# Optimization experiments

Measured on AMD Instinct MI355X. Metric: run time of the kernel, lower is better.

Reference implementation:

```python
import jax, jax.numpy as jnp
import numpy as np

NUM_CATS = 5
EPS = 1e-6


def setup_inputs() -> dict:
    key = jax.random.key(0)
    k1, k2, k3, k4 = jax.random.split(key, 4)
    B, C, H, W = 64, 3, 256, 256
    restored = jax.random.normal(k1, (B, C, H, W), dtype=jnp.float32)
    clean_patch_1 = jax.random.normal(k2, (B, C, H, W), dtype=jnp.float32)
    un = jax.random.uniform(k3, (B, C, H, W), dtype=jnp.float32)
    de_id = jax.random.randint(k4, (B,), 0, NUM_CATS)
    return {"restored": restored, "clean_patch_1": clean_patch_1,
            "de_id": de_id, "un": un}


def _loss(restored, clean, un, de_id):
    B, C, H, W = restored.shape
    E = C * H * W  # elements per sample
    dt = restored.dtype

    onehot = (de_id[:, None] == jnp.arange(NUM_CATS)[None, :])  # [B,5] bool
    m = onehot.astype(dt)                                        # [B,5]
    counts = onehot.sum(0)                                       # [5] int
    nonempty = counts > 0
    safe_counts = jnp.maximum(counts, 1).astype(dt)              # avoid 0-div

    # Per-category mean uncertainty map: un_map[c] = mean_{i: de_id[i]=c} un[i] + eps
    un_sum = jnp.einsum('bk,bchw->kchw', m, un)                  # [5,C,H,W]
    un_map = un_sum / safe_counts[:, None, None, None] + EPS     # [5,C,H,W]
    s = 1.0 / un_map                                             # [5,C,H,W]

    # Per-sample scaled L1 (s gathered by each sample's category)
    absdiff = jnp.abs(clean - restored)                          # [B,C,H,W]
    scaled_sum_per_sample = (absdiff * s[de_id]).sum(axis=(1, 2, 3))  # [B]
    abs_sum_per_sample = absdiff.sum(axis=(1, 2, 3))                  # [B]

    cat_scaled_sum = jnp.einsum('bk,b->k', m, scaled_sum_per_sample)  # [5]
    cat_abs_sum = jnp.einsum('bk,b->k', m, abs_sum_per_sample)        # [5]

    # NOTE: the original code never clears un_hq_list/un_lq_list between
    # categories, so the L1 at category c is the mean over ALL samples from
    # categories 0..c (each scaled by its OWN category's s). Replicate that
    # via cumulative sums/counts over the category axis.
    cum_scaled = jnp.cumsum(cat_scaled_sum)                      # [5]
    cum_elems = jnp.cumsum(counts).astype(dt) * E                # [5]
    cum_l1 = cum_scaled / jnp.maximum(cum_elems, 1.0)            # [5]

    old_loss = jnp.where(nonempty, cat_abs_sum / (safe_counts * E), 0.0)
    un_num = un_map.mean(axis=(1, 2, 3))                         # [5]
    bn = jnp.where(nonempty, 2.0 * jnp.log(un_num), 0.0)
    unc_l1 = jnp.where(nonempty, cum_l1, 0.0)

    cat_losses = unc_l1 + bn                                     # [5]
    num = nonempty.sum().astype(dt)
    total = cat_losses.sum() / num
    return total, cat_losses, old_loss, bn, unc_l1


def reference(restored, clean_patch_1, de_id, un):
    return _loss(restored, clean_patch_1, un, de_id)
```

## Files before the change

kernel.cpp:

```cpp
#include <hip/hip_runtime.h>
#include <math.h>

#define NCAT  5
#define BATCH 64
#define ELEMS 196608
#define P4    49152
#define EPSV  1e-6f

#define P1_TPB 64
#define P1_NBLK 768
#define P1_GRP 8

#define P2_PB  192
#define P2_SCH 8
#define P2_CHB (BATCH / P2_SCH)
#define P2_NCOL (P2_PB * P2_SCH)

#define NBLK 768
#define TPB  256
#define GRP  8

__global__ __launch_bounds__(P1_TPB) void phase1_kernel(
    const float4* __restrict__ un,
    const int*    __restrict__ de_id,
    float4*       __restrict__ rmap,
    float*        __restrict__ partials1)
{
    __shared__ int   sh_de[BATCH];
    __shared__ float sh_inv[NCAT];

    const int tid = threadIdx.x;
    {
        int k = de_id[tid];
        sh_de[tid] = k;
        #pragma unroll
        for (int j = 0; j < NCAT; ++j) {
            unsigned long long m = __ballot(k == j);
            if (tid == j) {
                int c = __popcll(m);
                sh_inv[j] = 1.0f / (float)(c > 0 ? c : 1);
            }
        }
    }
    __syncthreads();

    const int p4 = blockIdx.x * P1_TPB + tid;
    const float4* up = un + p4;

    float4 un_s[NCAT];
    #pragma unroll
    for (int j = 0; j < NCAT; ++j) un_s[j] = make_float4(0.f, 0.f, 0.f, 0.f);

    float4 ub[2][P1_GRP];
    #pragma unroll
    for (int i = 0; i < P1_GRP; ++i) ub[0][i] = up[(size_t)i * P4];

    #pragma unroll
    for (int g = 0; g < BATCH / P1_GRP; ++g) {
        const int cur = g & 1, nxt = cur ^ 1;
        if (g < BATCH / P1_GRP - 1) {
            #pragma unroll
            for (int i = 0; i < P1_GRP; ++i)
                ub[nxt][i] = up[(size_t)((g + 1) * P1_GRP + i) * P4];
        }
        #pragma unroll
        for (int i = 0; i < P1_GRP; ++i) {
            float4 u = ub[cur][i];
            int k = sh_de[g * P1_GRP + i];
            #pragma unroll
            for (int j = 0; j < NCAT; ++j) {
                float m = (k == j) ? 1.0f : 0.0f;
                un_s[j].x = fmaf(m, u.x, un_s[j].x);
                un_s[j].y = fmaf(m, u.y, un_s[j].y);
                un_s[j].z = fmaf(m, u.z, un_s[j].z);
                un_s[j].w = fmaf(m, u.w, un_s[j].w);
            }
        }
    }

    float vals[NCAT];
    #pragma unroll
    for (int j = 0; j < NCAT; ++j) {
        float inv = sh_inv[j];
        float4 r;
        r.x = 1.0f / fmaf(un_s[j].x, inv, EPSV);
        r.y = 1.0f / fmaf(un_s[j].y, inv, EPSV);
        r.z = 1.0f / fmaf(un_s[j].z, inv, EPSV);
        r.w = 1.0f / fmaf(un_s[j].w, inv, EPSV);
        rmap[(size_t)j * P4 + p4] = r;
        vals[j] = un_s[j].x + un_s[j].y + un_s[j].z + un_s[j].w;
    }

    #pragma unroll
    for (int j = 0; j < NCAT; ++j) {
        float v = vals[j];
        #pragma unroll
        for (int off = 32; off >= 1; off >>= 1)
            v += __shfl_down(v, off, 64);
        if (tid == 0) partials1[j * P1_NBLK + blockIdx.x] = v;
    }
}

__global__ __launch_bounds__(256) void phase2_kernel(
    const float4* __restrict__ restored,
    const float4* __restrict__ clean,
    const int*    __restrict__ de_id,
    const float4* __restrict__ rmap,
    float*        __restrict__ partials2)
{
    __shared__ int   sh_de[BATCH];
    __shared__ float sred[4][2 * NCAT];

    const int tid = threadIdx.x;
    if (tid < 64) sh_de[tid] = de_id[tid];
    __syncthreads();

    const int p4 = blockIdx.x * 256 + tid;
    const int b0 = blockIdx.y * P2_CHB;
    const float4* cp = clean + p4;
    const float4* rp = restored + p4;

    float4 ad4[NCAT];
    #pragma unroll
    for (int j = 0; j < NCAT; ++j) ad4[j] = make_float4(0.f, 0.f, 0.f, 0.f);

    float4 cb[2][2], rb[2][2];
    #pragma unroll
    for (int i = 0; i < 2; ++i) {
        const size_t off = (size_t)(b0 + i) * P4;
        cb[0][i] = cp[off];
        rb[0][i] = rp[off];
    }

    #pragma unroll
    for (int g = 0; g < P2_CHB / 2; ++g) {
        const int cur = g & 1, nxt = cur ^ 1;
        if (g < P2_CHB / 2 - 1) {
            #pragma unroll
            for (int i = 0; i < 2; ++i) {
                const size_t off = (size_t)(b0 + (g + 1) * 2 + i) * P4;
                cb[nxt][i] = cp[off];
                rb[nxt][i] = rp[off];
            }
        }
        #pragma unroll
        for (int i = 0; i < 2; ++i) {
            float4 c = cb[cur][i], r = rb[cur][i];
            float ax = fabsf(c.x - r.x);
            float ay = fabsf(c.y - r.y);
            float az = fabsf(c.z - r.z);
            float aw = fabsf(c.w - r.w);
            int k = sh_de[b0 + g * 2 + i];
            #pragma unroll
            for (int j = 0; j < NCAT; ++j) {
                float m = (k == j) ? 1.0f : 0.0f;
                ad4[j].x = fmaf(m, ax, ad4[j].x);
                ad4[j].y = fmaf(m, ay, ad4[j].y);
                ad4[j].z = fmaf(m, az, ad4[j].z);
                ad4[j].w = fmaf(m, aw, ad4[j].w);
            }
        }
    }

    float vals[2 * NCAT];
    #pragma unroll
    for (int j = 0; j < NCAT; ++j) {
        float4 m4 = rmap[(size_t)j * P4 + p4];
        vals[j] = ad4[j].x * m4.x + ad4[j].y * m4.y +
                  ad4[j].z * m4.z + ad4[j].w * m4.w;
        vals[NCAT + j] = ad4[j].x + ad4[j].y + ad4[j].z + ad4[j].w;
    }

    #pragma unroll
    for (int i = 0; i < 2 * NCAT; ++i) {
        float v = vals[i];
        #pragma unroll
        for (int off = 32; off >= 1; off >>= 1)
            v += __shfl_down(v, off, 64);
        vals[i] = v;
    }

    const int wave = tid >> 6, lane = tid & 63;
    if (lane == 0) {
        #pragma unroll
        for (int i = 0; i < 2 * NCAT; ++i) sred[wave][i] = vals[i];
    }
    __syncthreads();

    if (tid < 2 * NCAT) {
        float v = sred[0][tid] + sred[1][tid] + sred[2][tid] + sred[3][tid];
        const int col = blockIdx.y * P2_PB + blockIdx.x;
        partials2[tid * P2_NCOL + col] = v;
    }
}

__global__ __launch_bounds__(TPB) void accum_kernel(
    const float* __restrict__ restored,
    const float* __restrict__ clean,
    const int*   __restrict__ de_id,
    const float* __restrict__ un,
    float*       __restrict__ partials)
{
    __shared__ int   sh_de[BATCH];
    __shared__ float sh_inv[NCAT];
    __shared__ float sred[TPB / 64][3 * NCAT];

    const int tid = threadIdx.x;
    if (tid < 64) {
        int k = de_id[tid];
        sh_de[tid] = k;
        #pragma unroll
        for (int j = 0; j < NCAT; ++j) {
            unsigned long long m = __ballot(k == j);
            if (tid == j) {
                int c = __popcll(m);
                sh_inv[j] = 1.0f / (float)(c > 0 ? c : 1);
            }
        }
    }
    __syncthreads();

    const int p = blockIdx.x * TPB + tid;
    const float* rp = restored + p;
    const float* cp = clean + p;
    const float* up = un + p;

    float un_s[NCAT] = {0.f, 0.f, 0.f, 0.f, 0.f};
    float ad_s[NCAT] = {0.f, 0.f, 0.f, 0.f, 0.f};

    float ub[2][GRP], cb[2][GRP], rb[2][GRP];
    #pragma unroll
    for (int i = 0; i < GRP; ++i) {
        const size_t off = (size_t)i * ELEMS;
        ub[0][i] = up[off]; cb[0][i] = cp[off]; rb[0][i] = rp[off];
    }
    #pragma unroll
    for (int g = 0; g < BATCH / GRP; ++g) {
        const int cur = g & 1, nxt = cur ^ 1;
        if (g < BATCH / GRP - 1) {
            #pragma unroll
            for (int i = 0; i < GRP; ++i) {
                const size_t off = (size_t)((g + 1) * GRP + i) * ELEMS;
                ub[nxt][i] = up[off]; cb[nxt][i] = cp[off]; rb[nxt][i] = rp[off];
            }
        }
        #pragma unroll
        for (int i = 0; i < GRP; ++i) {
            float u  = ub[cur][i];
            float ad = fabsf(cb[cur][i] - rb[cur][i]);
            int   k  = sh_de[g * GRP + i];
            #pragma unroll
            for (int j = 0; j < NCAT; ++j) {
                float m = (k == j) ? 1.0f : 0.0f;
                un_s[j] = fmaf(m, u,  un_s[j]);
                ad_s[j] = fmaf(m, ad, ad_s[j]);
            }
        }
    }

    float vals[3 * NCAT];
    #pragma unroll
    for (int j = 0; j < NCAT; ++j) {
        float um = fmaf(un_s[j], sh_inv[j], EPSV);
        vals[j]            = ad_s[j] / um;
        vals[NCAT + j]     = ad_s[j];
        vals[2 * NCAT + j] = un_s[j];
    }
    #pragma unroll
    for (int i = 0; i < 3 * NCAT; ++i) {
        float v = vals[i];
        #pragma unroll
        for (int off = 32; off >= 1; off >>= 1)
            v += __shfl_down(v, off, 64);
        vals[i] = v;
    }
    const int wave = tid >> 6, lane = tid & 63;
    if (lane == 0) {
        #pragma unroll
        for (int i = 0; i < 3 * NCAT; ++i) sred[wave][i] = vals[i];
    }
    __syncthreads();
    if (tid < 3 * NCAT) {
        float v = sred[0][tid] + sred[1][tid] + sred[2][tid] + sred[3][tid];
        partials[tid * NBLK + blockIdx.x] = v;
    }
}

__global__ __launch_bounds__(256) void epilogue_kernel(
    const int*   __restrict__ de_id,
    const float* __restrict__ pSA, int nA,
    const float* __restrict__ pUN, int nB,
    float*       __restrict__ out)
{
    __shared__ int   sh_cnt[NCAT];
    __shared__ float sh_acc[3 * NCAT];

    const int tid = threadIdx.x;
    if (tid < 64) {
        int k = de_id[tid];
        #pragma unroll
        for (int j = 0; j < NCAT; ++j) {
            unsigned long long m = __ballot(k == j);
            if (tid == j) sh_cnt[j] = __popcll(m);
        }
    }

    if (tid < 240) {
        const int row    = tid >> 4;
        const int lane16 = tid & 15;
        const float* base = (row < 10) ? (pSA + row * nA) : (pUN + (row - 10) * nB);
        const int n = (row < 10) ? nA : nB;
        float v = 0.f;
        for (int k = lane16; k < n; k += 16) v += base[k];
        v += __shfl_down(v, 8, 16);
        v += __shfl_down(v, 4, 16);
        v += __shfl_down(v, 2, 16);
        v += __shfl_down(v, 1, 16);
        if (lane16 == 0) sh_acc[row] = v;
    }
    __syncthreads();

    if (tid == 0) {
        const float Ef = (float)ELEMS;
        float cum_s = 0.f;
        long  cum_c = 0;
        float total = 0.f;
        int   num   = 0;
        float cat_losses[NCAT], old_loss[NCAT], bn[NCAT], unc_l1[NCAT];

        for (int j = 0; j < NCAT; ++j) {
            cum_s += sh_acc[j];
            cum_c += sh_cnt[j];
            float cum_elems = (float)cum_c * Ef;
            float cum_l1    = cum_s / fmaxf(cum_elems, 1.0f);

            bool  ne   = sh_cnt[j] > 0;
            float safe = (float)(ne ? sh_cnt[j] : 1);

            old_loss[j]  = ne ? sh_acc[NCAT + j] / (safe * Ef) : 0.f;
            float un_num = sh_acc[2 * NCAT + j] / (safe * Ef) + EPSV;
            bn[j]        = ne ? 2.0f * logf(un_num) : 0.f;
            unc_l1[j]    = ne ? cum_l1 : 0.f;
            cat_losses[j] = unc_l1[j] + bn[j];
            total += cat_losses[j];
            num   += ne ? 1 : 0;
        }
        total /= (float)num;

        out[0] = total;
        for (int j = 0; j < NCAT; ++j) {
            out[1 + j]  = cat_losses[j];
            out[6 + j]  = old_loss[j];
            out[11 + j] = bn[j];
            out[16 + j] = unc_l1[j];
        }
    }
}

extern "C" void kernel_launch(void* const* d_in, const int* in_sizes, int n_in,
                              void* d_out, int out_size, void* d_ws, size_t ws_size,
                              hipStream_t stream) {
    (void)in_sizes; (void)n_in; (void)out_size;
    const float* restored = (const float*)d_in[0];
    const float* clean    = (const float*)d_in[1];
    const int*   de_id    = (const int*)d_in[2];
    const float* un       = (const float*)d_in[3];
    float* out = (float*)d_out;

    const size_t rmap_bytes = (size_t)NCAT * P4 * sizeof(float4);
    const size_t p1_bytes   = (size_t)NCAT * P1_NBLK * sizeof(float);
    const size_t p2_bytes   = (size_t)2 * NCAT * P2_NCOL * sizeof(float);

    if (ws_size >= rmap_bytes + p1_bytes + p2_bytes) {
        float4* rmap      = (float4*)d_ws;
        float*  partials1 = (float*)((char*)d_ws + rmap_bytes);
        float*  partials2 = (float*)((char*)d_ws + rmap_bytes + p1_bytes);

        phase1_kernel<<<P1_NBLK, P1_TPB, 0, stream>>>(
            (const float4*)un, de_id, rmap, partials1);
        phase2_kernel<<<dim3(P2_PB, P2_SCH), 256, 0, stream>>>(
            (const float4*)restored, (const float4*)clean, de_id,
            (const float4*)rmap, partials2);
        epilogue_kernel<<<1, 256, 0, stream>>>(
            de_id, partials2, P2_NCOL, partials1, P1_NBLK, out);
    } else {
        float* partials = (float*)d_ws;
        accum_kernel<<<NBLK, TPB, 0, stream>>>(restored, clean, de_id, un, partials);
        epilogue_kernel<<<1, 256, 0, stream>>>(
            de_id, partials, NBLK, partials + 10 * NBLK, NBLK, out);
    }
}
```

Baseline: 190.1 us.

## Split uncertainty reduction across batch chunks with separate reciprocal-map kernel

The per-category uncertainty sum was computed by 768 single-wave blocks that each walked all 64 samples. It is now split into 8 batch-chunk blocks per position tile, which write per-chunk partial maps. A new kernel sums those partials and forms the reciprocal map. The abs-diff pass is retiled so each thread handles two float4 positions per batch chunk. This exposes more parallelism to hide memory latency, at the cost of writing and re-reading the partial maps in the workspace and one extra kernel launch.

```diff
diff --git a/kernel.cpp b/kernel.cpp
--- a/kernel.cpp
+++ b/kernel.cpp
@@ -7,32 +7,115 @@
 #define P4    49152
 #define EPSV  1e-6f
 
-#define P1_TPB 64
-#define P1_NBLK 768
-#define P1_GRP 8
-
-#define P2_PB  192
-#define P2_SCH 8
-#define P2_CHB (BATCH / P2_SCH)
-#define P2_NCOL (P2_PB * P2_SCH)
+#define TILE4 512
+#define NPOSB 96
+#define BCH   8
+#define NCH   8
+#define NCOLS (NPOSB * NCH)
 
 #define NBLK 768
 #define TPB  256
 #define GRP  8
 
-__global__ __launch_bounds__(P1_TPB) void phase1_kernel(
+__device__ __forceinline__ float hsum4(const float4 v) {
+    return v.x + v.y + v.z + v.w;
+}
+__device__ __forceinline__ float dot4(const float4 a, const float4 b) {
+    return a.x * b.x + a.y * b.y + a.z * b.z + a.w * b.w;
+}
+
+__global__ __launch_bounds__(256) void un_pass_kernel(
     const float4* __restrict__ un,
     const int*    __restrict__ de_id,
-    float4*       __restrict__ rmap,
-    float*        __restrict__ partials1)
+    float4*       __restrict__ unpart,
+    float*        __restrict__ unblk)
 {
-    __shared__ int   sh_de[BATCH];
+    __shared__ int   sh_de[BCH];
+    __shared__ float sred[4][NCAT];
+
+    const int tid = threadIdx.x;
+    const int pb  = blockIdx.x;
+    const int ch  = blockIdx.y;
+    if (tid < BCH) sh_de[tid] = de_id[ch * BCH + tid];
+    __syncthreads();
+
+    const int p0 = pb * TILE4 + tid;
+    const float4* up = un + p0;
+
+    float4 un_s[2][NCAT];
+    #pragma unroll
+    for (int s = 0; s < 2; ++s)
+        #pragma unroll
+        for (int j = 0; j < NCAT; ++j)
+            un_s[s][j] = make_float4(0.f, 0.f, 0.f, 0.f);
+
+    float4 ub[2][2];
+    #pragma unroll
+    for (int s = 0; s < 2; ++s)
+        ub[0][s] = up[(size_t)(ch * BCH) * P4 + (s << 8)];
+
+    #pragma unroll
+    for (int b = 0; b < BCH; ++b) {
+        const int cur = b & 1, nxt = cur ^ 1;
+        if (b < BCH - 1) {
+            #pragma unroll
+            for (int s = 0; s < 2; ++s)
+                ub[nxt][s] = up[(size_t)(ch * BCH + b + 1) * P4 + (s << 8)];
+        }
+        const int k = sh_de[b];
+        #pragma unroll
+        for (int j = 0; j < NCAT; ++j) {
+            const float m = (k == j) ? 1.0f : 0.0f;
+            #pragma unroll
+            for (int s = 0; s < 2; ++s) {
+                un_s[s][j].x = fmaf(m, ub[cur][s].x, un_s[s][j].x);
+                un_s[s][j].y = fmaf(m, ub[cur][s].y, un_s[s][j].y);
+                un_s[s][j].z = fmaf(m, ub[cur][s].z, un_s[s][j].z);
+                un_s[s][j].w = fmaf(m, ub[cur][s].w, un_s[s][j].w);
+            }
+        }
+    }
+
+    #pragma unroll
+    for (int j = 0; j < NCAT; ++j)
+        #pragma unroll
+        for (int s = 0; s < 2; ++s)
+            unpart[(size_t)(ch * NCAT + j) * P4 + p0 + (s << 8)] = un_s[s][j];
+
+    float vals[NCAT];
+    #pragma unroll
+    for (int j = 0; j < NCAT; ++j)
+        vals[j] = hsum4(un_s[0][j]) + hsum4(un_s[1][j]);
+
+    #pragma unroll
+    for (int j = 0; j < NCAT; ++j) {
+        float v = vals[j];
+        #pragma unroll
+        for (int off = 32; off >= 1; off >>= 1)
+            v += __shfl_down(v, off, 64);
+        vals[j] = v;
+    }
+    const int wave = tid >> 6, lane = tid & 63;
+    if (lane == 0) {
+        #pragma unroll
+        for (int j = 0; j < NCAT; ++j) sred[wave][j] = vals[j];
+    }
+    __syncthreads();
+    if (tid < NCAT) {
+        float v = sred[0][tid] + sred[1][tid] + sred[2][tid] + sred[3][tid];
+        unblk[tid * NCOLS + ch * NPOSB + pb] = v;
+    }
+}
+
+__global__ __launch_bounds__(256) void rmap_kernel(
+    const int*    __restrict__ de_id,
+    const float4* __restrict__ unpart,
+    float4*       __restrict__ rmap)
+{
     __shared__ float sh_inv[NCAT];
-
     const int tid = threadIdx.x;
-    {
+    if (tid < 64) {
         int k = de_id[tid];
-        sh_de[tid] = k;
         #pragma unroll
         for (int j = 0; j < NCAT; ++j) {
             unsigned long long m = __ballot(k == j);
@@ -44,120 +127,84 @@
     }
     __syncthreads();
 
-    const int p4 = blockIdx.x * P1_TPB + tid;
-    const float4* up = un + p4;
-
-    float4 un_s[NCAT];
-    #pragma unroll
-    for (int j = 0; j < NCAT; ++j) un_s[j] = make_float4(0.f, 0.f, 0.f, 0.f);
-
-    float4 ub[2][P1_GRP];
-    #pragma unroll
-    for (int i = 0; i < P1_GRP; ++i) ub[0][i] = up[(size_t)i * P4];
-
-    #pragma unroll
-    for (int g = 0; g < BATCH / P1_GRP; ++g) {
-        const int cur = g & 1, nxt = cur ^ 1;
-        if (g < BATCH / P1_GRP - 1) {
-            #pragma unroll
-            for (int i = 0; i < P1_GRP; ++i)
-                ub[nxt][i] = up[(size_t)((g + 1) * P1_GRP + i) * P4];
-        }
-        #pragma unroll
-        for (int i = 0; i < P1_GRP; ++i) {
-            float4 u = ub[cur][i];
-            int k = sh_de[g * P1_GRP + i];
-            #pragma unroll
-            for (int j = 0; j < NCAT; ++j) {
-                float m = (k == j) ? 1.0f : 0.0f;
-                un_s[j].x = fmaf(m, u.x, un_s[j].x);
-                un_s[j].y = fmaf(m, u.y, un_s[j].y);
-                un_s[j].z = fmaf(m, u.z, un_s[j].z);
-                un_s[j].w = fmaf(m, u.w, un_s[j].w);
-            }
-        }
-    }
-
-    float vals[NCAT];
-    #pragma unroll
-    for (int j = 0; j < NCAT; ++j) {
-        float inv = sh_inv[j];
-        float4 r;
-        r.x = 1.0f / fmaf(un_s[j].x, inv, EPSV);
-        r.y = 1.0f / fmaf(un_s[j].y, inv, EPSV);
-        r.z = 1.0f / fmaf(un_s[j].z, inv, EPSV);
-        r.w = 1.0f / fmaf(un_s[j].w, inv, EPSV);
-        rmap[(size_t)j * P4 + p4] = r;
-        vals[j] = un_s[j].x + un_s[j].y + un_s[j].z + un_s[j].w;
-    }
-
-    #pragma unroll
-    for (int j = 0; j < NCAT; ++j) {
-        float v = vals[j];
-        #pragma unroll
-        for (int off = 32; off >= 1; off >>= 1)
-            v += __shfl_down(v, off, 64);
-        if (tid == 0) partials1[j * P1_NBLK + blockIdx.x] = v;
-    }
-}
-
-__global__ __launch_bounds__(256) void phase2_kernel(
+    const int p4  = blockIdx.x * 256 + tid;
+    const int cat = blockIdx.y;
+
+    float4 s = make_float4(0.f, 0.f, 0.f, 0.f);
+    #pragma unroll
+    for (int ch = 0; ch < NCH; ++ch) {
+        float4 v = unpart[(size_t)(ch * NCAT + cat) * P4 + p4];
+        s.x += v.x; s.y += v.y; s.z += v.z; s.w += v.w;
+    }
+    const float inv = sh_inv[cat];
+    float4 r;
+    r.x = 1.0f / fmaf(s.x, inv, EPSV);
+    r.y = 1.0f / fmaf(s.y, inv, EPSV);
+    r.z = 1.0f / fmaf(s.z, inv, EPSV);
+    r.w = 1.0f / fmaf(s.w, inv, EPSV);
+    rmap[(size_t)cat * P4 + p4] = r;
+}
+
+__global__ __launch_bounds__(256) void ad_pass_kernel(
     const float4* __restrict__ restored,
     const float4* __restrict__ clean,
+    const float4* __restrict__ rmap,
     const int*    __restrict__ de_id,
-    const float4* __restrict__ rmap,
-    float*        __restrict__ partials2)
+    float*        __restrict__ part2)
 {
-    __shared__ int   sh_de[BATCH];
+    __shared__ int   sh_de[BCH];
     __shared__ float sred[4][2 * NCAT];
 
     const int tid = threadIdx.x;
-    if (tid < 64) sh_de[tid] = de_id[tid];
-    __syncthreads();
-
-    const int p4 = blockIdx.x * 256 + tid;
-    const int b0 = blockIdx.y * P2_CHB;
-    const float4* cp = clean + p4;
-    const float4* rp = restored + p4;
-
-    float4 ad4[NCAT];
-    #pragma unroll
-    for (int j = 0; j < NCAT; ++j) ad4[j] = make_float4(0.f, 0.f, 0.f, 0.f);
+    const int pb  = blockIdx.x;
+    const int ch  = blockIdx.y;
+    if (tid < BCH) sh_de[tid] = de_id[ch * BCH + tid];
+    __syncthreads();
+
+    const int p0 = pb * TILE4 + tid;
+    const float4* cp = clean + p0;
+    const float4* rp = restored + p0;
+
+    float4 ad_s[2][NCAT];
+    #pragma unroll
+    for (int s = 0; s < 2; ++s)
+        #pragma unroll
+        for (int j = 0; j < NCAT; ++j)
+            ad_s[s][j] = make_float4(0.f, 0.f, 0.f, 0.f);
 
     float4 cb[2][2], rb[2][2];
     #pragma unroll
-    for (int i = 0; i < 2; ++i) {
-        const size_t off = (size_t)(b0 + i) * P4;
-        cb[0][i] = cp[off];
-        rb[0][i] = rp[off];
-    }
-
-    #pragma unroll
-    for (int g = 0; g < P2_CHB / 2; ++g) {
-        const int cur = g & 1, nxt = cur ^ 1;
-        if (g < P2_CHB / 2 - 1) {
-            #pragma unroll
-            for (int i = 0; i < 2; ++i) {
-                const size_t off = (size_t)(b0 + (g + 1) * 2 + i) * P4;
-                cb[nxt][i] = cp[off];
-                rb[nxt][i] = rp[off];
-            }
-        }
-        #pragma unroll
-        for (int i = 0; i < 2; ++i) {
-            float4 c = cb[cur][i], r = rb[cur][i];
-            float ax = fabsf(c.x - r.x);
-            float ay = fabsf(c.y - r.y);
-            float az = fabsf(c.z - r.z);
-            float aw = fabsf(c.w - r.w);
-            int k = sh_de[b0 + g * 2 + i];
+    for (int s = 0; s < 2; ++s) {
+        const size_t off = (size_t)(ch * BCH) * P4 + (s << 8);
+        cb[0][s] = cp[off];
+        rb[0][s] = rp[off];
+    }
+
+    #pragma unroll
+    for (int b = 0; b < BCH; ++b) {
+        const int cur = b & 1, nxt = cur ^ 1;
+        if (b < BCH - 1) {
+            #pragma unroll
+            for (int s = 0; s < 2; ++s) {
+                const size_t off = (size_t)(ch * BCH + b + 1) * P4 + (s << 8);
+                cb[nxt][s] = cp[off];
+                rb[nxt][s] = rp[off];
+            }
+        }
+        const int k = sh_de[b];
+        #pragma unroll
+        for (int s = 0; s < 2; ++s) {
+            float ax = fabsf(cb[cur][s].x - rb[cur][s].x);
+            float ay = fabsf(cb[cur][s].y - rb[cur][s].y);
+            float az = fabsf(cb[cur][s].z - rb[cur][s].z);
+            float aw = fabsf(cb[cur][s].w - rb[cur][s].w);
             #pragma unroll
             for (int j = 0; j < NCAT; ++j) {
-                float m = (k == j) ? 1.0f : 0.0f;
-                ad4[j].x = fmaf(m, ax, ad4[j].x);
-                ad4[j].y = fmaf(m, ay, ad4[j].y);
-                ad4[j].z = fmaf(m, az, ad4[j].z);
-                ad4[j].w = fmaf(m, aw, ad4[j].w);
+                const float m = (k == j) ? 1.0f : 0.0f;
+                ad_s[s][j].x = fmaf(m, ax, ad_s[s][j].x);
+                ad_s[s][j].y = fmaf(m, ay, ad_s[s][j].y);
+                ad_s[s][j].z = fmaf(m, az, ad_s[s][j].z);
+                ad_s[s][j].w = fmaf(m, aw, ad_s[s][j].w);
             }
         }
     }
@@ -165,10 +212,10 @@
     float vals[2 * NCAT];
     #pragma unroll
     for (int j = 0; j < NCAT; ++j) {
-        float4 m4 = rmap[(size_t)j * P4 + p4];
-        vals[j] = ad4[j].x * m4.x + ad4[j].y * m4.y +
-                  ad4[j].z * m4.z + ad4[j].w * m4.w;
-        vals[NCAT + j] = ad4[j].x + ad4[j].y + ad4[j].z + ad4[j].w;
+        float4 m0 = rmap[(size_t)j * P4 + p0];
+        float4 m1 = rmap[(size_t)j * P4 + p0 + 256];
+        vals[j]        = dot4(ad_s[0][j], m0) + dot4(ad_s[1][j], m1);
+        vals[NCAT + j] = hsum4(ad_s[0][j]) + hsum4(ad_s[1][j]);
     }
 
     #pragma unroll
@@ -179,18 +226,15 @@
             v += __shfl_down(v, off, 64);
         vals[i] = v;
     }
-
     const int wave = tid >> 6, lane = tid & 63;
     if (lane == 0) {
         #pragma unroll
         for (int i = 0; i < 2 * NCAT; ++i) sred[wave][i] = vals[i];
     }
     __syncthreads();
-
     if (tid < 2 * NCAT) {
         float v = sred[0][tid] + sred[1][tid] + sred[2][tid] + sred[3][tid];
-        const int col = blockIdx.y * P2_PB + blockIdx.x;
-        partials2[tid * P2_NCOL + col] = v;
+        part2[tid * NCOLS + ch * NPOSB + pb] = v;
     }
 }
 
@@ -367,22 +411,25 @@
     const float* un       = (const float*)d_in[3];
     float* out = (float*)d_out;
 
-    const size_t rmap_bytes = (size_t)NCAT * P4 * sizeof(float4);
-    const size_t p1_bytes   = (size_t)NCAT * P1_NBLK * sizeof(float);
-    const size_t p2_bytes   = (size_t)2 * NCAT * P2_NCOL * sizeof(float);
-
-    if (ws_size >= rmap_bytes + p1_bytes + p2_bytes) {
-        float4* rmap      = (float4*)d_ws;
-        float*  partials1 = (float*)((char*)d_ws + rmap_bytes);
-        float*  partials2 = (float*)((char*)d_ws + rmap_bytes + p1_bytes);
-
-        phase1_kernel<<<P1_NBLK, P1_TPB, 0, stream>>>(
-            (const float4*)un, de_id, rmap, partials1);
-        phase2_kernel<<<dim3(P2_PB, P2_SCH), 256, 0, stream>>>(
-            (const float4*)restored, (const float4*)clean, de_id,
-            (const float4*)rmap, partials2);
+    const size_t unpart_b = (size_t)NCH * NCAT * P4 * sizeof(float4);
+    const size_t rmap_b   = (size_t)NCAT * P4 * sizeof(float4);
+    const size_t unblk_b  = (size_t)NCAT * NCOLS * sizeof(float);
+    const size_t part2_b  = (size_t)10 * NCOLS * sizeof(float);
+
+    if (ws_size >= unpart_b + rmap_b + unblk_b + part2_b) {
+        float4* unpart = (float4*)d_ws;
+        float4* rmap   = (float4*)((char*)d_ws + unpart_b);
+        float*  unblk  = (float*)((char*)d_ws + unpart_b + rmap_b);
+        float*  part2  = (float*)((char*)d_ws + unpart_b + rmap_b + unblk_b);
+
+        un_pass_kernel<<<dim3(NPOSB, NCH), 256, 0, stream>>>(
+            (const float4*)un, de_id, unpart, unblk);
+        rmap_kernel<<<dim3(P4 / 256, NCAT), 256, 0, stream>>>(
+            de_id, unpart, rmap);
+        ad_pass_kernel<<<dim3(NPOSB, NCH), 256, 0, stream>>>(
+            (const float4*)restored, (const float4*)clean, rmap, de_id, part2);
         epilogue_kernel<<<1, 256, 0, stream>>>(
-            de_id, partials2, P2_NCOL, partials1, P1_NBLK, out);
+            de_id, part2, NCOLS, unblk, NCOLS, out);
     } else {
         float* partials = (float*)d_ws;
         accum_kernel<<<NBLK, TPB, 0, stream>>>(restored, clean, de_id, un, partials);
```

Result: no change. 190.6 us (+0.3%).
